# Performance work log

Hardware: AMD Instinct MI355X
Metric: run time of the kernel (lower is better)

The kernel has to match this reference:

```python
import jax, jax.numpy as jnp
import numpy as np

B, C, H, W = 4, 512, 64, 64
INTER = 64  # C // channel_stride


def setup_inputs() -> dict:
    key = jax.random.key(0)
    ks = jax.random.split(key, 5)
    s = 0.02  # small init scale for numerical stability of softmax logits
    return {
        "inputs": jax.random.normal(ks[0], (B, C, H, W), dtype=jnp.float32),
        "Wq": jax.random.normal(ks[1], (INTER, C), dtype=jnp.float32) * s,
        "bq": jnp.zeros((INTER,), dtype=jnp.float32),
        "Wk": jax.random.normal(ks[2], (INTER, C), dtype=jnp.float32) * s,
        "bk": jnp.zeros((INTER,), dtype=jnp.float32),
        "Wv": jax.random.normal(ks[3], (C, C), dtype=jnp.float32) * s,
        "bv": jnp.zeros((C,), dtype=jnp.float32),
        "gamma": jax.random.normal(ks[4], (1,), dtype=jnp.float32),
    }


def reference(inputs, Wq, bq, Wk, bk, Wv, bv, gamma):
    b, c, h, w = inputs.shape
    n = h * w
    x = inputs.reshape(b, c, n)  # (B, C, N)
    # 1x1 convs == per-pixel linear projections
    q = jnp.einsum('dc,bcn->bnd', Wq, x) + bq            # (B, N, d)
    k = jnp.einsum('dc,bcn->bdn', Wk, x) + bk[:, None]   # (B, d, N)
    v = jnp.einsum('oc,bcn->bon', Wv, x) + bv[:, None]   # (B, O, N)
    # affinity: (B, Nq, Nk), softmax over keys (last dim), no scaling (as in source)
    affinity = jax.nn.softmax(jnp.einsum('bnd,bdm->bnm', q, k), axis=-1)
    # note: torch does bmm(value, affinity) -> out[b,o,m] = sum_j v[b,o,j] * A[b,j,m]
    out = jnp.einsum('bon,bnm->bom', v, affinity)        # (B, O, N)
    return gamma * out.reshape(b, -1, h, w) + inputs
```

## Files before the change

kernel.cpp:

```cpp
#include <hip/hip_runtime.h>
#include <stdint.h>

typedef __attribute__((ext_vector_type(8))) short short8;
typedef __attribute__((ext_vector_type(4))) float f32x4;
typedef __attribute__((ext_vector_type(8))) unsigned short u16x8;
typedef __attribute__((ext_vector_type(4))) unsigned short u16x4;
typedef __attribute__((ext_vector_type(2))) unsigned short u16x2;
typedef unsigned short u16;

#define NPIX 4096
#define CCH  512
#define DD   64


__device__ inline float b2f(u16 h){
  union { unsigned int i; float f; } u; u.i = ((unsigned int)h) << 16; return u.f;
}
__device__ inline u16 f2b(float f){
  union { float f; unsigned int i; } u; u.f = f;
  return (u16)((u.i + 0x7fffu + ((u.i >> 16) & 1u)) >> 16);
}
__device__ inline void gl2lds16(const void* g, void* l){
  __builtin_amdgcn_global_load_lds((const __attribute__((address_space(1))) unsigned int*)g,
                                   (__attribute__((address_space(3))) unsigned int*)l, 16, 0, 0);
}
__device__ inline f32x4 mfma16(short8 a, short8 b, f32x4 c){
  return __builtin_amdgcn_mfma_f32_16x16x32_bf16(a, b, c, 0, 0, 0);
}

__global__ __launch_bounds__(256) void k_cvt(const float* __restrict__ src,
                                             u16* __restrict__ dst, int n){
  int i = blockIdx.x * 256 + threadIdx.x;
  if (i < n){
    int row = i >> 9, col = i & 511;
    dst[(row << 9) + (col ^ ((row & 7) << 3))] = f2b(src[i]);
  }
}

__global__ __launch_bounds__(256) void k0_transpose(const float* __restrict__ x,
                                                    u16* __restrict__ xT){
  __shared__ u16 tile[64][66];
  const int b = blockIdx.z;
  const int n0 = blockIdx.x * 64, c0 = blockIdx.y * 64;
  const float* xb = x + ((size_t)b * CCH + c0) * NPIX + n0;
  #pragma unroll
  for (int r = 0; r < 16; ++r){
    int id = r * 256 + threadIdx.x;
    int cc = id >> 6, nn = id & 63;
    tile[nn][cc] = f2b(xb[(size_t)cc * NPIX + nn]);
  }
  __syncthreads();
  u16* xTb = xT + ((size_t)b * NPIX + n0) * CCH + c0;
  #pragma unroll
  for (int r = 0; r < 8; ++r){
    int id = r * 256 + threadIdx.x;
    int nn = id >> 5, c2 = id & 31;
    int colp = (2 * c2) ^ ((nn & 7) << 3);
    *(u16x2*)(xTb + (size_t)nn * CCH + colp) = *(const u16x2*)&tile[nn][2 * c2];
  }
}

__global__ __launch_bounds__(256) void k1_qk(const u16* __restrict__ xT,
    const u16* __restrict__ Wqk, const float* __restrict__ bq,
    const float* __restrict__ bk, u16* __restrict__ Qb, u16* __restrict__ Kb){
  __shared__ __align__(16) u16 As[128*64];
  __shared__ __align__(16) u16 Bs[128*64];
  const int b  = blockIdx.z;
  const int n0 = blockIdx.x * 128;
  const u16* Ab = xT + ((size_t)b * NPIX + n0) * CCH;
  const int t = threadIdx.x, wave = t >> 6, lane = t & 63, q = lane >> 4, l16 = lane & 15;
  const int wr = (wave >> 1) * 64, wc = (wave & 1) * 64;
  const int sw = l16 & 7;
  f32x4 acc[4][4];
  #pragma unroll
  for (int i = 0; i < 4; ++i)
    #pragma unroll
    for (int j = 0; j < 4; ++j) acc[i][j] = (f32x4){0.f,0.f,0.f,0.f};

  for (int k0 = 0; k0 < CCH; k0 += 64){
    __syncthreads();
    #pragma unroll
    for (int r = 0; r < 4; ++r){
      int id = r * 256 + t;
      int row = id >> 3, ko = (id & 7) << 3;
      gl2lds16(Ab + (size_t)row * CCH + k0 + ko, &As[id * 8]);
      gl2lds16(Wqk + (size_t)row * CCH + k0 + ko, &Bs[id * 8]);
    }
    __syncthreads();
    #pragma unroll
    for (int s = 0; s < 2; ++s){
      const int ca = ((s*4 + q) ^ sw) << 3;
      short8 af[4], bfr[4];
      #pragma unroll
      for (int i = 0; i < 4; ++i){
        af[i]  = *(const short8*)&As[(wr + i*16 + l16)*64 + ca];
        bfr[i] = *(const short8*)&Bs[(wc + i*16 + l16)*64 + ca];
      }
      #pragma unroll
      for (int i = 0; i < 4; ++i)
        #pragma unroll
        for (int j = 0; j < 4; ++j)
          acc[i][j] = mfma16(af[i], bfr[j], acc[i][j]);
    }
  }
  #pragma unroll
  for (int i = 0; i < 4; ++i){
    #pragma unroll
    for (int j = 0; j < 4; ++j){
      int col = wc + j*16 + l16;
      #pragma unroll
      for (int r2 = 0; r2 < 4; ++r2){
        int n = n0 + wr + i*16 + q*4 + r2;
        int sw8 = (n & 7) << 3;
        float v = acc[i][j][r2];
        if (col < 64) Qb[((size_t)b * NPIX + n) * DD + (col ^ sw8)]        = f2b(v + bq[col]);
        else          Kb[((size_t)b * NPIX + n) * DD + ((col - 64) ^ sw8)] = f2b(v + bk[col - 64]);
      }
    }
  }
}

__global__ __launch_bounds__(256) void k2_v(const u16* __restrict__ xT,
    const u16* __restrict__ Wvb, const float* __restrict__ bv, u16* __restrict__ Vb){
  __shared__ __align__(16) u16 As[128*64];
  __shared__ __align__(16) u16 Bs[128*64];
  const int b  = blockIdx.z;
  const int n0 = blockIdx.x * 128;
  const int o0 = blockIdx.y * 128;
  const u16* Ab = Wvb + (size_t)o0 * CCH;
  const u16* Bb = xT + ((size_t)b * NPIX + n0) * CCH;
  const int t = threadIdx.x, wave = t >> 6, lane = t & 63, q = lane >> 4, l16 = lane & 15;
  const int wr = (wave >> 1) * 64, wc = (wave & 1) * 64;
  const int sw = l16 & 7;
  f32x4 acc[4][4];
  #pragma unroll
  for (int i = 0; i < 4; ++i)
    #pragma unroll
    for (int j = 0; j < 4; ++j) acc[i][j] = (f32x4){0.f,0.f,0.f,0.f};

  for (int k0 = 0; k0 < CCH; k0 += 64){
    __syncthreads();
    #pragma unroll
    for (int r = 0; r < 4; ++r){
      int id = r * 256 + t;
      int row = id >> 3, ko = (id & 7) << 3;
      gl2lds16(Ab + (size_t)row * CCH + k0 + ko, &As[id * 8]);
      gl2lds16(Bb + (size_t)row * CCH + k0 + ko, &Bs[id * 8]);
    }
    __syncthreads();
    #pragma unroll
    for (int s = 0; s < 2; ++s){
      const int ca = ((s*4 + q) ^ sw) << 3;
      short8 af[4], bfr[4];
      #pragma unroll
      for (int i = 0; i < 4; ++i){
        af[i]  = *(const short8*)&As[(wr + i*16 + l16)*64 + ca];
        bfr[i] = *(const short8*)&Bs[(wc + i*16 + l16)*64 + ca];
      }
      #pragma unroll
      for (int i = 0; i < 4; ++i)
        #pragma unroll
        for (int j = 0; j < 4; ++j)
          acc[i][j] = mfma16(af[i], bfr[j], acc[i][j]);
    }
  }
  #pragma unroll
  for (int i = 0; i < 4; ++i){
    #pragma unroll
    for (int j = 0; j < 4; ++j){
      int n = n0 + wc + j*16 + l16;
      #pragma unroll
      for (int r2 = 0; r2 < 4; ++r2){
        int o = o0 + wr + i*16 + q*4 + r2;
        int np = n ^ ((o & 7) << 3);
        Vb[((size_t)b * CCH + o) * NPIX + np] = f2b(acc[i][j][r2] + bv[o]);
      }
    }
  }
}

__global__ __launch_bounds__(256) void k3_logits(const u16* __restrict__ Qb,
    const u16* __restrict__ Kb, u16* __restrict__ E, float* __restrict__ Z, int b0){
  __shared__ __align__(16) u16 smem[128*136];
  u16* As = smem;
  u16* Bs = smem + 128*64;
  const int bloc = blockIdx.z, b = b0 + bloc;
  const int n0 = blockIdx.x * 128;
  const int m0 = blockIdx.y * 128;
  const u16* Ab = Kb + ((size_t)b * NPIX + m0) * DD;
  const u16* Bb = Qb + ((size_t)b * NPIX + n0) * DD;
  const int t = threadIdx.x, wave = t >> 6, lane = t & 63, q = lane >> 4, l16 = lane & 15;
  const int wr = (wave >> 1) * 64, wc = (wave & 1) * 64;
  const int sw = l16 & 7;
  f32x4 acc[4][4];
  #pragma unroll
  for (int i = 0; i < 4; ++i)
    #pragma unroll
    for (int j = 0; j < 4; ++j) acc[i][j] = (f32x4){0.f,0.f,0.f,0.f};

  #pragma unroll
  for (int r = 0; r < 4; ++r){
    int id = r * 256 + t;
    int row = id >> 3, ko = (id & 7) << 3;
    gl2lds16(Ab + row * DD + ko, &As[id * 8]);
    gl2lds16(Bb + row * DD + ko, &Bs[id * 8]);
  }
  __syncthreads();
  #pragma unroll
  for (int s = 0; s < 2; ++s){
    const int ca = ((s*4 + q) ^ sw) << 3;
    short8 af[4], bfr[4];
    #pragma unroll
    for (int i = 0; i < 4; ++i){
      af[i]  = *(const short8*)&As[(wr + i*16 + l16)*64 + ca];
      bfr[i] = *(const short8*)&Bs[(wc + i*16 + l16)*64 + ca];
    }
    #pragma unroll
    for (int i = 0; i < 4; ++i)
      #pragma unroll
      for (int j = 0; j < 4; ++j)
        acc[i][j] = mfma16(af[i], bfr[j], acc[i][j]);
  }
  __syncthreads();
  u16* tile = smem;
  float colsum[4] = {0.f, 0.f, 0.f, 0.f};
  #pragma unroll
  for (int i = 0; i < 4; ++i){
    #pragma unroll
    for (int j = 0; j < 4; ++j){
      #pragma unroll
      for (int r2 = 0; r2 < 4; ++r2){
        int mrow = wr + i*16 + q*4 + r2;
        int ncol = wc + j*16 + l16;
        float l = fminf(fmaxf(acc[i][j][r2], -60.f), 30.f);
        float e = __expf(l);
        tile[mrow * 136 + ncol] = f2b(e);
        colsum[j] += e;
      }
    }
  }
  #pragma unroll
  for (int j = 0; j < 4; ++j){
    float v = colsum[j];
    v += __shfl_xor(v, 16, 64);
    v += __shfl_xor(v, 32, 64);
    if (q == 0) atomicAdd(&Z[(size_t)b * NPIX + n0 + wc + j*16 + l16], v);
  }
  __syncthreads();
  u16* Eb = E + (size_t)bloc * NPIX * NPIX;
  #pragma unroll
  for (int r = 0; r < 8; ++r){
    int id = r * 256 + t;
    int row = id >> 4, chunk = id & 15;
    int g = chunk >> 3, c3 = chunk & 7;
    int colp = g * 64 + ((c3 ^ (row & 7)) << 3);
    *(u16x8*)(Eb + (size_t)(m0 + row) * NPIX + n0 + colp) =
        *(const u16x8*)&tile[row * 136 + chunk * 8];
  }
}

__global__ __launch_bounds__(256) void k3b_scale(u16* __restrict__ Vb,
    const float* __restrict__ Z, const float* __restrict__ gm, int b0){
  size_t i4  = ((size_t)blockIdx.x * 256 + threadIdx.x) * 4;
  size_t off = ((size_t)b0 << 21) + i4;
  int b = (int)(off >> 21);
  int o = (int)((off >> 12) & 511);
  int np = (int)(off & (NPIX - 1));
  int nl = np ^ ((o & 7) << 3);
  float g = gm[0];
  u16x4 vv = *(const u16x4*)(Vb + off);
  f32x4 zz = *(const f32x4*)(Z + ((size_t)b << 12) + nl);
  u16x4 r;
  #pragma unroll
  for (int k = 0; k < 4; ++k) r[k] = f2b(g * b2f(vv[k]) / fmaxf(zz[k], 1e-20f));
  *(u16x4*)(Vb + off) = r;
}

__global__ __launch_bounds__(256) void k4_out(const u16* __restrict__ Vs,
    const u16* __restrict__ E, const float* __restrict__ xin,
    float* __restrict__ outp, int b0){
  __shared__ __align__(16) u16 As[128*64];
  __shared__ __align__(16) u16 Bs[128*64];
  const int bloc = blockIdx.z, b = b0 + bloc;
  const int m0 = blockIdx.x * 128;
  const int o0 = blockIdx.y * 128;
  const u16* Ab = Vs + ((size_t)b * CCH + o0) * NPIX;
  const u16* Bb = E + (size_t)bloc * NPIX * NPIX + (size_t)m0 * NPIX;
  const int t = threadIdx.x, wave = t >> 6, lane = t & 63, q = lane >> 4, l16 = lane & 15;
  const int wr = (wave >> 1) * 64, wc = (wave & 1) * 64;
  const int sw = l16 & 7;
  f32x4 acc[4][4];
  #pragma unroll
  for (int i = 0; i < 4; ++i)
    #pragma unroll
    for (int j = 0; j < 4; ++j) acc[i][j] = (f32x4){0.f,0.f,0.f,0.f};

  for (int k0 = 0; k0 < NPIX; k0 += 64){
    __syncthreads();
    #pragma unroll
    for (int r = 0; r < 4; ++r){
      int id = r * 256 + t;
      int row = id >> 3, ko = (id & 7) << 3;
      gl2lds16(Ab + (size_t)row * NPIX + k0 + ko, &As[id * 8]);
      gl2lds16(Bb + (size_t)row * NPIX + k0 + ko, &Bs[id * 8]);
    }
    __syncthreads();
    #pragma unroll
    for (int s = 0; s < 2; ++s){
      const int ca = ((s*4 + q) ^ sw) << 3;
      short8 af[4], bfr[4];
      #pragma unroll
      for (int i = 0; i < 4; ++i){
        af[i]  = *(const short8*)&As[(wr + i*16 + l16)*64 + ca];
        bfr[i] = *(const short8*)&Bs[(wc + i*16 + l16)*64 + ca];
      }
      #pragma unroll
      for (int i = 0; i < 4; ++i)
        #pragma unroll
        for (int j = 0; j < 4; ++j)
          acc[i][j] = mfma16(af[i], bfr[j], acc[i][j]);
    }
  }
  const float* xb = xin + (size_t)b * CCH * NPIX;
  float* ob = outp + (size_t)b * CCH * NPIX;
  #pragma unroll
  for (int i = 0; i < 4; ++i){
    #pragma unroll
    for (int j = 0; j < 4; ++j){
      int m = m0 + wc + j*16 + l16;
      #pragma unroll
      for (int r2 = 0; r2 < 4; ++r2){
        int o = o0 + wr + i*16 + q*4 + r2;
        size_t idx = (size_t)o * NPIX + m;
        ob[idx] = acc[i][j][r2] + xb[idx];
      }
    }
  }
}

extern "C" void kernel_launch(void* const* d_in, const int* in_sizes, int n_in,
                              void* d_out, int out_size, void* d_ws, size_t ws_size,
                              hipStream_t stream){
  (void)in_sizes; (void)n_in; (void)out_size;
  const float* x  = (const float*)d_in[0];
  const float* Wq = (const float*)d_in[1];
  const float* bq = (const float*)d_in[2];
  const float* Wk = (const float*)d_in[3];
  const float* bk = (const float*)d_in[4];
  const float* Wv = (const float*)d_in[5];
  const float* bv = (const float*)d_in[6];
  const float* gm = (const float*)d_in[7];
  float* outp = (float*)d_out;

  char* ws = (char*)d_ws;
  u16*  Qb   = (u16*)(ws + 0);
  u16*  Kb   = (u16*)(ws + 2097152);
  u16*  Vb   = (u16*)(ws + 4194304);
  float* Z   = (float*)(ws + 20971520);
  u16*  Wqkb = (u16*)(ws + 21037056);
  u16*  Wvb  = (u16*)(ws + 21168128);
  u16*  xT   = (u16*)(ws + 21692416);
  u16*  E    = (u16*)(ws + 21692416);

  const size_t ebytes = (size_t)NPIX * NPIX * 2;
  const size_t base   = 21692416;
  if (ws_size < base + ebytes){
    return;
  }
  int NB = 1;
  if (ws_size >= base + 4 * ebytes) NB = 4;
  else if (ws_size >= base + 2 * ebytes) NB = 2;

  hipMemsetAsync(Z, 0, (size_t)4 * NPIX * sizeof(float), stream);
  k_cvt<<<dim3(128), 256, 0, stream>>>(Wq, Wqkb, 32768);
  k_cvt<<<dim3(128), 256, 0, stream>>>(Wk, Wqkb + 32768, 32768);
  k_cvt<<<dim3(1024), 256, 0, stream>>>(Wv, Wvb, 262144);
  k0_transpose<<<dim3(64, 8, 4), 256, 0, stream>>>(x, xT);
  k1_qk<<<dim3(32, 1, 4), 256, 0, stream>>>(xT, Wqkb, bq, bk, Qb, Kb);
  k2_v<<<dim3(32, 4, 4), 256, 0, stream>>>(xT, Wvb, bv, Vb);
  for (int b0 = 0; b0 < 4; b0 += NB){
    int nb = NB; if (b0 + nb > 4) nb = 4 - b0;
    k3_logits<<<dim3(32, 32, nb), 256, 0, stream>>>(Qb, Kb, E, Z, b0);
    k3b_scale<<<dim3(nb * 2048), 256, 0, stream>>>(Vb, Z, gm, b0);
    k4_out<<<dim3(32, 4, nb), 256, 0, stream>>>(Vb, E, x, outp, b0);
  }
}
```

Baseline: 251.5 us.

## Fuse logits exp into output GEMM, eliminating materialized affinity matrix

Replaces the write-then-read of the full bf16 exp(logits) matrix with on-the-fly recomputation inside the output GEMM kernel, keeping each exp tile in shared memory. The denominator pass now only accumulates column sums without storing E. This removes a large HBM round trip per batch. In exchange, logits are recomputed once per output-channel tile, shared memory use grows, and each chunk needs more barriers. The two weight-conversion launches are also merged.

```diff
diff --git a/kernel.cpp b/kernel.cpp
--- a/kernel.cpp
+++ b/kernel.cpp
@@ -3,7 +3,6 @@
 
 typedef __attribute__((ext_vector_type(8))) short short8;
 typedef __attribute__((ext_vector_type(4))) float f32x4;
-typedef __attribute__((ext_vector_type(8))) unsigned short u16x8;
 typedef __attribute__((ext_vector_type(4))) unsigned short u16x4;
 typedef __attribute__((ext_vector_type(2))) unsigned short u16x2;
 typedef unsigned short u16;
@@ -28,13 +27,19 @@
   return __builtin_amdgcn_mfma_f32_16x16x32_bf16(a, b, c, 0, 0, 0);
 }
 
-__global__ __launch_bounds__(256) void k_cvt(const float* __restrict__ src,
-                                             u16* __restrict__ dst, int n){
+__global__ __launch_bounds__(256) void k_cvt_qk(const float* __restrict__ Wq,
+    const float* __restrict__ Wk, u16* __restrict__ dst){
   int i = blockIdx.x * 256 + threadIdx.x;
-  if (i < n){
-    int row = i >> 9, col = i & 511;
-    dst[(row << 9) + (col ^ ((row & 7) << 3))] = f2b(src[i]);
-  }
+  int row = i >> 9, col = i & 511;
+  float v = (row < 64) ? Wq[(row << 9) + col] : Wk[((row - 64) << 9) + col];
+  dst[(row << 9) + (col ^ ((row & 7) << 3))] = f2b(v);
+}
+
+__global__ __launch_bounds__(256) void k_cvt_v(const float* __restrict__ src,
+                                               u16* __restrict__ dst){
+  int i = blockIdx.x * 256 + threadIdx.x;
+  int row = i >> 9, col = i & 511;
+  dst[(row << 9) + (col ^ ((row & 7) << 3))] = f2b(src[i]);
 }
 
 __global__ __launch_bounds__(256) void k0_transpose(const float* __restrict__ x,
@@ -179,12 +184,11 @@
   }
 }
 
-__global__ __launch_bounds__(256) void k3_logits(const u16* __restrict__ Qb,
-    const u16* __restrict__ Kb, u16* __restrict__ E, float* __restrict__ Z, int b0){
-  __shared__ __align__(16) u16 smem[128*136];
-  u16* As = smem;
-  u16* Bs = smem + 128*64;
-  const int bloc = blockIdx.z, b = b0 + bloc;
+__global__ __launch_bounds__(256) void k3z_denom(const u16* __restrict__ Qb,
+    const u16* __restrict__ Kb, float* __restrict__ Z){
+  __shared__ __align__(16) u16 As[128*64];
+  __shared__ __align__(16) u16 Bs[128*64];
+  const int b  = blockIdx.z;
   const int n0 = blockIdx.x * 128;
   const int m0 = blockIdx.y * 128;
   const u16* Ab = Kb + ((size_t)b * NPIX + m0) * DD;
@@ -221,24 +225,16 @@
       for (int j = 0; j < 4; ++j)
         acc[i][j] = mfma16(af[i], bfr[j], acc[i][j]);
   }
-  __syncthreads();
-  u16* tile = smem;
   float colsum[4] = {0.f, 0.f, 0.f, 0.f};
   #pragma unroll
-  for (int i = 0; i < 4; ++i){
-    #pragma unroll
-    for (int j = 0; j < 4; ++j){
+  for (int i = 0; i < 4; ++i)
+    #pragma unroll
+    for (int j = 0; j < 4; ++j)
       #pragma unroll
       for (int r2 = 0; r2 < 4; ++r2){
-        int mrow = wr + i*16 + q*4 + r2;
-        int ncol = wc + j*16 + l16;
         float l = fminf(fmaxf(acc[i][j][r2], -60.f), 30.f);
-        float e = __expf(l);
-        tile[mrow * 136 + ncol] = f2b(e);
-        colsum[j] += e;
-      }
-    }
-  }
+        colsum[j] += __expf(l);
+      }
   #pragma unroll
   for (int j = 0; j < 4; ++j){
     float v = colsum[j];
@@ -246,23 +242,11 @@
     v += __shfl_xor(v, 32, 64);
     if (q == 0) atomicAdd(&Z[(size_t)b * NPIX + n0 + wc + j*16 + l16], v);
   }
-  __syncthreads();
-  u16* Eb = E + (size_t)bloc * NPIX * NPIX;
-  #pragma unroll
-  for (int r = 0; r < 8; ++r){
-    int id = r * 256 + t;
-    int row = id >> 4, chunk = id & 15;
-    int g = chunk >> 3, c3 = chunk & 7;
-    int colp = g * 64 + ((c3 ^ (row & 7)) << 3);
-    *(u16x8*)(Eb + (size_t)(m0 + row) * NPIX + n0 + colp) =
-        *(const u16x8*)&tile[row * 136 + chunk * 8];
-  }
 }
 
 __global__ __launch_bounds__(256) void k3b_scale(u16* __restrict__ Vb,
-    const float* __restrict__ Z, const float* __restrict__ gm, int b0){
-  size_t i4  = ((size_t)blockIdx.x * 256 + threadIdx.x) * 4;
-  size_t off = ((size_t)b0 << 21) + i4;
+    const float* __restrict__ Z, const float* __restrict__ gm){
+  size_t off = ((size_t)blockIdx.x * 256 + threadIdx.x) * 4;
   int b = (int)(off >> 21);
   int o = (int)((off >> 12) & 511);
   int np = (int)(off & (NPIX - 1));
@@ -276,43 +260,96 @@
   *(u16x4*)(Vb + off) = r;
 }
 
-__global__ __launch_bounds__(256) void k4_out(const u16* __restrict__ Vs,
-    const u16* __restrict__ E, const float* __restrict__ xin,
-    float* __restrict__ outp, int b0){
-  __shared__ __align__(16) u16 As[128*64];
-  __shared__ __align__(16) u16 Bs[128*64];
-  const int bloc = blockIdx.z, b = b0 + bloc;
+__global__ __launch_bounds__(256) void k4_fused(const u16* __restrict__ Qb,
+    const u16* __restrict__ Kb, const u16* __restrict__ Vb,
+    const float* __restrict__ xin, float* __restrict__ outp){
+  __shared__ __align__(16) u16 Ks [128*64];
+  __shared__ __align__(16) u16 Qs [64*64];
+  __shared__ __align__(16) u16 Vss[128*64];
+  __shared__ __align__(16) u16 Ps [128*64];
+  const int b  = blockIdx.z;
   const int m0 = blockIdx.x * 128;
   const int o0 = blockIdx.y * 128;
-  const u16* Ab = Vs + ((size_t)b * CCH + o0) * NPIX;
-  const u16* Bb = E + (size_t)bloc * NPIX * NPIX + (size_t)m0 * NPIX;
   const int t = threadIdx.x, wave = t >> 6, lane = t & 63, q = lane >> 4, l16 = lane & 15;
   const int wr = (wave >> 1) * 64, wc = (wave & 1) * 64;
   const int sw = l16 & 7;
+  const int wm = wave * 32;
+
+  const u16* Kbase = Kb + ((size_t)b * NPIX + m0) * DD;
+  #pragma unroll
+  for (int r = 0; r < 4; ++r){
+    int id = r * 256 + t;
+    int row = id >> 3, ko = (id & 7) << 3;
+    gl2lds16(Kbase + row * DD + ko, &Ks[id * 8]);
+  }
+
   f32x4 acc[4][4];
   #pragma unroll
   for (int i = 0; i < 4; ++i)
     #pragma unroll
     for (int j = 0; j < 4; ++j) acc[i][j] = (f32x4){0.f,0.f,0.f,0.f};
 
-  for (int k0 = 0; k0 < NPIX; k0 += 64){
-    __syncthreads();
+  for (int ch = 0; ch < 64; ++ch){
+    const int nb = ch * 64;
+    __syncthreads();
+    const u16* Qbase = Qb + ((size_t)b * NPIX + nb) * DD;
+    #pragma unroll
+    for (int r = 0; r < 2; ++r){
+      int id = r * 256 + t;
+      int row = id >> 3, ko = (id & 7) << 3;
+      gl2lds16(Qbase + row * DD + ko, &Qs[id * 8]);
+    }
+    const u16* Vbase = Vb + ((size_t)b * CCH + o0) * NPIX + nb;
     #pragma unroll
     for (int r = 0; r < 4; ++r){
       int id = r * 256 + t;
       int row = id >> 3, ko = (id & 7) << 3;
-      gl2lds16(Ab + (size_t)row * NPIX + k0 + ko, &As[id * 8]);
-      gl2lds16(Bb + (size_t)row * NPIX + k0 + ko, &Bs[id * 8]);
-    }
-    __syncthreads();
+      gl2lds16(Vbase + (size_t)row * NPIX + ko, &Vss[id * 8]);
+    }
+    __syncthreads();
+
+    f32x4 accs[2][4];
+    #pragma unroll
+    for (int i = 0; i < 2; ++i)
+      #pragma unroll
+      for (int j = 0; j < 4; ++j) accs[i][j] = (f32x4){0.f,0.f,0.f,0.f};
+    #pragma unroll
+    for (int kd = 0; kd < 2; ++kd){
+      const int ca = ((kd*4 + q) ^ sw) << 3;
+      short8 ak[2], aq[4];
+      #pragma unroll
+      for (int i = 0; i < 2; ++i) ak[i] = *(const short8*)&Ks[(wm + i*16 + l16)*64 + ca];
+      #pragma unroll
+      for (int j = 0; j < 4; ++j) aq[j] = *(const short8*)&Qs[(j*16 + l16)*64 + ca];
+      #pragma unroll
+      for (int i = 0; i < 2; ++i)
+        #pragma unroll
+        for (int j = 0; j < 4; ++j)
+          accs[i][j] = mfma16(ak[i], aq[j], accs[i][j]);
+    }
+    #pragma unroll
+    for (int i = 0; i < 2; ++i){
+      #pragma unroll
+      for (int j = 0; j < 4; ++j){
+        #pragma unroll
+        for (int r2 = 0; r2 < 4; ++r2){
+          int ml = wm + i*16 + q*4 + r2;
+          int nl = j*16 + l16;
+          float l = fminf(fmaxf(accs[i][j][r2], -60.f), 30.f);
+          Ps[ml*64 + (((nl >> 3) ^ (ml & 7)) << 3) + (nl & 7)] = f2b(__expf(l));
+        }
+      }
+    }
+    __syncthreads();
+
     #pragma unroll
     for (int s = 0; s < 2; ++s){
       const int ca = ((s*4 + q) ^ sw) << 3;
       short8 af[4], bfr[4];
       #pragma unroll
       for (int i = 0; i < 4; ++i){
-        af[i]  = *(const short8*)&As[(wr + i*16 + l16)*64 + ca];
-        bfr[i] = *(const short8*)&Bs[(wc + i*16 + l16)*64 + ca];
+        af[i]  = *(const short8*)&Vss[(wr + i*16 + l16)*64 + ca];
+        bfr[i] = *(const short8*)&Ps [(wc + i*16 + l16)*64 + ca];
       }
       #pragma unroll
       for (int i = 0; i < 4; ++i)
@@ -321,6 +358,7 @@
           acc[i][j] = mfma16(af[i], bfr[j], acc[i][j]);
     }
   }
+
   const float* xb = xin + (size_t)b * CCH * NPIX;
   float* ob = outp + (size_t)b * CCH * NPIX;
   #pragma unroll
@@ -360,28 +398,17 @@
   u16*  Wqkb = (u16*)(ws + 21037056);
   u16*  Wvb  = (u16*)(ws + 21168128);
   u16*  xT   = (u16*)(ws + 21692416);
-  u16*  E    = (u16*)(ws + 21692416);
-
-  const size_t ebytes = (size_t)NPIX * NPIX * 2;
-  const size_t base   = 21692416;
-  if (ws_size < base + ebytes){
+  if (ws_size < 38469632){
     return;
   }
-  int NB = 1;
-  if (ws_size >= base + 4 * ebytes) NB = 4;
-  else if (ws_size >= base + 2 * ebytes) NB = 2;
 
   hipMemsetAsync(Z, 0, (size_t)4 * NPIX * sizeof(float), stream);
-  k_cvt<<<dim3(128), 256, 0, stream>>>(Wq, Wqkb, 32768);
-  k_cvt<<<dim3(128), 256, 0, stream>>>(Wk, Wqkb + 32768, 32768);
-  k_cvt<<<dim3(1024), 256, 0, stream>>>(Wv, Wvb, 262144);
+  k_cvt_qk<<<dim3(256), 256, 0, stream>>>(Wq, Wk, Wqkb);
+  k_cvt_v<<<dim3(1024), 256, 0, stream>>>(Wv, Wvb);
   k0_transpose<<<dim3(64, 8, 4), 256, 0, stream>>>(x, xT);
   k1_qk<<<dim3(32, 1, 4), 256, 0, stream>>>(xT, Wqkb, bq, bk, Qb, Kb);
   k2_v<<<dim3(32, 4, 4), 256, 0, stream>>>(xT, Wvb, bv, Vb);
-  for (int b0 = 0; b0 < 4; b0 += NB){
-    int nb = NB; if (b0 + nb > 4) nb = 4 - b0;
-    k3_logits<<<dim3(32, 32, nb), 256, 0, stream>>>(Qb, Kb, E, Z, b0);
-    k3b_scale<<<dim3(nb * 2048), 256, 0, stream>>>(Vb, Z, gm, b0);
-    k4_out<<<dim3(32, 4, nb), 256, 0, stream>>>(Vb, E, x, outp, b0);
-  }
-}
+  k3z_denom<<<dim3(32, 32, 4), 256, 0, stream>>>(Qb, Kb, Z);
+  k3b_scale<<<dim3(8192), 256, 0, stream>>>(Vb, Z, gm);
+  k4_fused<<<dim3(32, 4, 4), 256, 0, stream>>>(Qb, Kb, Vb, x, outp);
+}
```

After: 317.8 us. +26.4%, slower.
